# Kernel optimization log

Hardware: AMD Instinct MI355X
Metric: run time of the kernel (lower is better)

The kernel has to match this reference:

```python
import jax, jax.numpy as jnp
import numpy as np

N_NODES = 50000
N_EDGES = 800000
NEG_SLOPE = 0.2  # PyG GATConv default negative_slope


def gat_conv(x, W, att_src, att_dst, bias, src, dst, heads, out_ch, concat):
    """PyG GATConv (eval mode, self-loops already appended to src/dst)."""
    n = x.shape[0]
    xh = (x @ W).reshape(n, heads, out_ch)            # [N,H,C]
    a_s = jnp.einsum('nhc,hc->nh', xh, att_src)       # [N,H]
    a_d = jnp.einsum('nhc,hc->nh', xh, att_dst)
    e = a_s[src] + a_d[dst]                           # [E,H]
    e = jnp.where(e > 0, e, NEG_SLOPE * e)            # LeakyReLU
    # segment softmax over incoming edges of each target node (dst)
    m = jax.ops.segment_max(e, dst, num_segments=n)
    e = jnp.exp(e - m[dst])
    denom = jax.ops.segment_sum(e, dst, num_segments=n)
    alpha = e / (denom[dst] + 1e-16)                  # [E,H]
    msg = xh[src] * alpha[:, :, None]                 # [E,H,C]
    out = jax.ops.segment_sum(msg, dst, num_segments=n)  # [N,H,C]
    out = out.reshape(n, heads * out_ch) if concat else out.mean(axis=1)
    return out + bias


def setup_inputs() -> dict:
    key = jax.random.key(0)
    ks = jax.random.split(key, 16)
    x = jax.random.normal(ks[0], (N_NODES, 256), dtype=jnp.float32)
    edge_index = jax.random.randint(ks[1], (2, N_EDGES), 0, N_NODES, dtype=jnp.int32)
    s = 0.05
    return {
        'x': x, 'edge_index': edge_index,
        'W0': jax.random.normal(ks[2], (256, 256), jnp.float32) * s,
        'as0': jax.random.normal(ks[3], (4, 64), jnp.float32) * s,
        'ad0': jax.random.normal(ks[4], (4, 64), jnp.float32) * s,
        'b0': jnp.zeros((256,), jnp.float32),
        'W1': jax.random.normal(ks[5], (256, 256), jnp.float32) * s,
        'as1': jax.random.normal(ks[6], (4, 64), jnp.float32) * s,
        'ad1': jax.random.normal(ks[7], (4, 64), jnp.float32) * s,
        'b1': jnp.zeros((256,), jnp.float32),
        'W2': jax.random.normal(ks[8], (256, 256), jnp.float32) * s,
        'as2': jax.random.normal(ks[9], (1, 256), jnp.float32) * s,
        'ad2': jax.random.normal(ks[10], (1, 256), jnp.float32) * s,
        'b2': jnp.zeros((256,), jnp.float32),
    }


def reference(x, edge_index, W0, as0, ad0, b0, W1, as1, ad1, b1, W2, as2, ad2, b2):
    # PyG GATConv adds self-loops by default
    loops = jnp.arange(x.shape[0], dtype=edge_index.dtype)
    src = jnp.concatenate([edge_index[0], loops])
    dst = jnp.concatenate([edge_index[1], loops])
    h = jax.nn.elu(gat_conv(x, W0, as0, ad0, b0, src, dst, 4, 64, True))
    h = jax.nn.elu(gat_conv(h, W1, as1, ad1, b1, src, dst, 4, 64, True))
    return gat_conv(h, W2, as2, ad2, b2, src, dst, 1, 256, False)
```

## Files before the change

kernel.cpp:

```cpp
#include <hip/hip_runtime.h>
#include <hip/hip_bf16.h>
#include <hip/hip_fp16.h>

#define N_NODES 50000
#define N_EDGES 800000
#define E_TOTAL (N_EDGES + N_NODES)
#define BKT 96

typedef _Float16 f16x8 __attribute__((ext_vector_type(8)));
typedef _Float16 f16x4 __attribute__((ext_vector_type(4)));
typedef float f32x4 __attribute__((ext_vector_type(4)));

__device__ __forceinline__ void gl_lds16(const _Float16* g, _Float16* l) {
  __builtin_amdgcn_global_load_lds(
      (const __attribute__((address_space(1))) unsigned int*)g,
      (__attribute__((address_space(3))) unsigned int*)l, 16, 0, 0);
}

#define XCAST_BLK (N_NODES * 256 / 8 / 256)
#define EDGE_BLK ((E_TOTAL + 255) / 256)
__global__ __launch_bounds__(256) void prep_kernel(
    const float* __restrict__ W0, const float* __restrict__ W1,
    const float* __restrict__ W2, const float* __restrict__ x,
    const int* __restrict__ ei, _Float16* __restrict__ WT0,
    _Float16* __restrict__ WT1, _Float16* __restrict__ WT2,
    _Float16* __restrict__ X16, int* __restrict__ cursor,
    int* __restrict__ csr_src) {
  __shared__ float tile[32][33];
  const int bid = blockIdx.x;
  if (bid < 192) {
    const float* W = (bid < 64) ? W0 : (bid < 128) ? W1 : W2;
    _Float16* WT = (bid < 64) ? WT0 : (bid < 128) ? WT1 : WT2;
    const int sub = bid & 63;
    const int bx = (sub & 7) * 32, by = (sub >> 3) * 32;
    const int tx = threadIdx.x & 31, ty = threadIdx.x >> 5;
#pragma unroll
    for (int i = 0; i < 32; i += 8)
      tile[ty + i][tx] = W[(size_t)(by + ty + i) * 256 + bx + tx];
    __syncthreads();
#pragma unroll
    for (int i = 0; i < 32; i += 8)
      WT[(size_t)(bx + ty + i) * 256 + by + tx] = (_Float16)tile[tx][ty + i];
  } else if (bid < 192 + XCAST_BLK) {
    size_t i = ((size_t)(bid - 192) * 256 + threadIdx.x) * 8;
    float4 u0 = *(const float4*)(x + i);
    float4 u1 = *(const float4*)(x + i + 4);
    f16x8 v;
    v[0] = (_Float16)u0.x; v[1] = (_Float16)u0.y;
    v[2] = (_Float16)u0.z; v[3] = (_Float16)u0.w;
    v[4] = (_Float16)u1.x; v[5] = (_Float16)u1.y;
    v[6] = (_Float16)u1.z; v[7] = (_Float16)u1.w;
    *(f16x8*)(X16 + i) = v;
  } else {
    int e = (bid - 192 - XCAST_BLK) * 256 + threadIdx.x;
    if (e < E_TOTAL) {
      int s, d;
      if (e < N_EDGES) {
        s = ei[e];
        d = ei[N_EDGES + e];
      } else {
        s = d = e - N_EDGES;
      }
      int pos = atomicAdd(&cursor[d], 1);
      csr_src[(size_t)d * BKT + pos] = s;
    }
  }
}

template <int H>
__global__ __launch_bounds__(256) void gemm_att(
    const _Float16* __restrict__ A, const _Float16* __restrict__ WT,
    const float* __restrict__ att_s, const float* __restrict__ att_d,
    _Float16* __restrict__ C, float* __restrict__ a_s, float* __restrict__ a_d,
    int M) {
  __shared__ _Float16 As[2][64 * 32];
  __shared__ _Float16 Bs[2][256 * 32];
  const int t = threadIdx.x, lane = t & 63, w = t >> 6;
  const int wr = w & 1, wc = w >> 1;
  const int row0 = blockIdx.x * 64;
  const int fr = lane & 15, fg = lane >> 4;
  const int srow = lane >> 2, sk = (lane & 3) * 8;

  f32x4 acc[2][8] = {};
  int cur = 0;

#define STAGE(buf, k0)                                                        \
  do {                                                                        \
    gl_lds16(A + (size_t)(row0 + w * 16 + srow) * 256 + (k0) + sk,            \
             &As[buf][w * 512]);                                              \
    gl_lds16(WT + (size_t)(w * 64 + srow) * 256 + (k0) + sk,                  \
             &Bs[buf][w * 2048]);                                             \
    gl_lds16(WT + (size_t)(w * 64 + 16 + srow) * 256 + (k0) + sk,             \
             &Bs[buf][w * 2048 + 512]);                                       \
    gl_lds16(WT + (size_t)(w * 64 + 32 + srow) * 256 + (k0) + sk,             \
             &Bs[buf][w * 2048 + 1024]);                                      \
    gl_lds16(WT + (size_t)(w * 64 + 48 + srow) * 256 + (k0) + sk,             \
             &Bs[buf][w * 2048 + 1536]);                                      \
  } while (0)

  STAGE(0, 0);
  __syncthreads();

  for (int kt = 0; kt < 8; kt++) {
    if (kt < 7) STAGE(cur ^ 1, (kt + 1) * 32);
    f16x8 af[2], bf[8];
#pragma unroll
    for (int mi = 0; mi < 2; mi++)
      af[mi] = *(const f16x8*)&As[cur][(wr * 32 + mi * 16 + fr) * 32 + fg * 8];
#pragma unroll
    for (int ni = 0; ni < 8; ni++)
      bf[ni] = *(const f16x8*)&Bs[cur][(wc * 128 + ni * 16 + fr) * 32 + fg * 8];
#pragma unroll
    for (int mi = 0; mi < 2; mi++)
#pragma unroll
      for (int ni = 0; ni < 8; ni++)
        acc[mi][ni] = __builtin_amdgcn_mfma_f32_16x16x32_f16(af[mi], bf[ni], acc[mi][ni], 0, 0, 0);
    __syncthreads();
    cur ^= 1;
  }
#undef STAGE

  float as_c[8], ad_c[8];
#pragma unroll
  for (int ni = 0; ni < 8; ni++) {
    int c = wc * 128 + ni * 16 + fr;
    as_c[ni] = att_s[c];
    ad_c[ni] = att_d[c];
  }

#pragma unroll
  for (int mi = 0; mi < 2; mi++) {
#pragma unroll
    for (int reg = 0; reg < 4; reg++) {
      const int r = row0 + wr * 32 + mi * 16 + fg * 4 + reg;
      const bool valid = r < M;
      if (valid) {
#pragma unroll
        for (int ni = 0; ni < 8; ni++)
          C[(size_t)r * 256 + wc * 128 + ni * 16 + fr] = (_Float16)acc[mi][ni][reg];
      }
      float s0 = 0.f, s1 = 0.f, d0 = 0.f, d1 = 0.f;
#pragma unroll
      for (int ni = 0; ni < 4; ni++) {
        s0 = fmaf(acc[mi][ni][reg], as_c[ni], s0);
        d0 = fmaf(acc[mi][ni][reg], ad_c[ni], d0);
        s1 = fmaf(acc[mi][ni + 4][reg], as_c[ni + 4], s1);
        d1 = fmaf(acc[mi][ni + 4][reg], ad_c[ni + 4], d1);
      }
#pragma unroll
      for (int off = 1; off < 16; off <<= 1) {
        s0 += __shfl_xor(s0, off, 64);
        d0 += __shfl_xor(d0, off, 64);
        s1 += __shfl_xor(s1, off, 64);
        d1 += __shfl_xor(d1, off, 64);
      }
      if constexpr (H == 4) {
        if (fr == 0 && valid) {
          a_s[(size_t)r * 4 + wc * 2 + 0] = s0;
          a_s[(size_t)r * 4 + wc * 2 + 1] = s1;
          a_d[(size_t)r * 4 + wc * 2 + 0] = d0;
          a_d[(size_t)r * 4 + wc * 2 + 1] = d1;
        }
      } else {
        if (fr == 0) {
          float* L = (float*)As;
          L[(r - row0) * 4 + wc * 2 + 0] = s0 + s1;
          L[(r - row0) * 4 + wc * 2 + 1] = d0 + d1;
        }
      }
    }
  }
  if constexpr (H == 1) {
    __syncthreads();
    float* L = (float*)As;
    if (t < 64 && row0 + t < M) {
      a_s[row0 + t] = L[t * 4 + 0] + L[t * 4 + 2];
      a_d[row0 + t] = L[t * 4 + 1] + L[t * 4 + 3];
    }
  }
}

template <int H, bool ELU_OUT, bool OUT_F16>
__global__ __launch_bounds__(256, 8) void aggregate_kernel(
    const _Float16* __restrict__ XH16, const float* __restrict__ a_s,
    const float* __restrict__ a_d, const int* __restrict__ cursor,
    const int* __restrict__ csr_src, const float* __restrict__ bias,
    void* __restrict__ outp) {
  const int t = threadIdx.x;
  const int lane = t & 63, w = t >> 6;
  const int d = blockIdx.x * 4 + w;
  const size_t e0 = (size_t)d * BKT;
  const int deg = cursor[d];
  const int li = lane & 15;
  const int h4 = (H == 4) ? (lane >> 4) : 0;
  const float adv = (H == 4) ? a_d[(size_t)d * 4 + h4] : a_d[d];

  float dnp = 0.f;
  float acc0 = 0.f, acc1 = 0.f, acc2 = 0.f, acc3 = 0.f;
  for (int base = 0; base < deg; base += 16) {
    const int cnt = min(16, deg - base);
    int s_cur = 0;
    float p = 0.f;
    if (li < cnt) {
      s_cur = csr_src[e0 + base + li];
      float e = ((H == 4) ? a_s[(size_t)s_cur * 4 + h4] : a_s[s_cur]) + adv;
      e = e > 0.f ? e : 0.2f * e;
      p = __expf(e);
    }
    dnp += p;
#define GAT_BODY(j)                                                           \
  {                                                                           \
    int sj = __builtin_amdgcn_readfirstlane(__shfl(s_cur, (j), 64));          \
    float alj = __shfl(p, (lane & 48) + (j), 64);                             \
    f16x4 raw = *(const f16x4*)(XH16 + (size_t)sj * 256 + lane * 4);          \
    acc0 = fmaf(alj, (float)raw[0], acc0);                                    \
    acc1 = fmaf(alj, (float)raw[1], acc1);                                    \
    acc2 = fmaf(alj, (float)raw[2], acc2);                                    \
    acc3 = fmaf(alj, (float)raw[3], acc3);                                    \
  }
    if (cnt == 16) {
#pragma unroll
      for (int j = 0; j < 16; j++) GAT_BODY(j)
    } else {
      for (int j = 0; j < cnt; j++) GAT_BODY(j)
    }
#undef GAT_BODY
  }
#pragma unroll
  for (int off = 1; off < 16; off <<= 1) dnp += __shfl_xor(dnp, off, 64);
  const float inv = 1.f / (dnp + 1e-16f);

  float4 bv = *(const float4*)&bias[lane * 4];
  float v0 = fmaf(acc0, inv, bv.x), v1 = fmaf(acc1, inv, bv.y);
  float v2 = fmaf(acc2, inv, bv.z), v3 = fmaf(acc3, inv, bv.w);
  if constexpr (ELU_OUT) {
    v0 = v0 > 0.f ? v0 : (__expf(v0) - 1.f);
    v1 = v1 > 0.f ? v1 : (__expf(v1) - 1.f);
    v2 = v2 > 0.f ? v2 : (__expf(v2) - 1.f);
    v3 = v3 > 0.f ? v3 : (__expf(v3) - 1.f);
  }
  if constexpr (OUT_F16) {
    _Float16* out = (_Float16*)outp;
    f16x4 ov;
    ov[0] = (_Float16)v0; ov[1] = (_Float16)v1;
    ov[2] = (_Float16)v2; ov[3] = (_Float16)v3;
    *(f16x4*)(out + (size_t)d * 256 + lane * 4) = ov;
  } else {
    float* out = (float*)outp;
    *(float4*)(out + (size_t)d * 256 + lane * 4) = make_float4(v0, v1, v2, v3);
  }
}

extern "C" void kernel_launch(void* const* d_in, const int* in_sizes, int n_in,
                              void* d_out, int out_size, void* d_ws, size_t ws_size,
                              hipStream_t stream) {
  const float* x = (const float*)d_in[0];
  const int* ei = (const int*)d_in[1];
  const float* W0 = (const float*)d_in[2];
  const float* as0 = (const float*)d_in[3];
  const float* ad0 = (const float*)d_in[4];
  const float* b0 = (const float*)d_in[5];
  const float* W1 = (const float*)d_in[6];
  const float* as1 = (const float*)d_in[7];
  const float* ad1 = (const float*)d_in[8];
  const float* b1 = (const float*)d_in[9];
  const float* W2 = (const float*)d_in[10];
  const float* as2 = (const float*)d_in[11];
  const float* ad2 = (const float*)d_in[12];
  const float* b2 = (const float*)d_in[13];
  float* out = (float*)d_out;

  char* p = (char*)d_ws;
  _Float16* XH16 = (_Float16*)p;
  p += (size_t)N_NODES * 256 * 2;
  _Float16* H16 = (_Float16*)p;
  p += (size_t)N_NODES * 256 * 2;
  _Float16* WT0 = (_Float16*)p;
  p += 256 * 256 * 2;
  _Float16* WT1 = (_Float16*)p;
  p += 256 * 256 * 2;
  _Float16* WT2 = (_Float16*)p;
  p += 256 * 256 * 2;
  float* a_s = (float*)p;
  p += (size_t)N_NODES * 4 * 4;
  float* a_d = (float*)p;
  p += (size_t)N_NODES * 4 * 4;
  int* cursor = (int*)p;
  p += (size_t)N_NODES * 4;
  int* csr_src = (int*)p;
  p += (size_t)N_NODES * BKT * 4;

  hipMemsetAsync(cursor, 0, (size_t)N_NODES * 4, stream);

  prep_kernel<<<192 + XCAST_BLK + EDGE_BLK, 256, 0, stream>>>(
      W0, W1, W2, x, ei, WT0, WT1, WT2, H16, cursor, csr_src);

  const int ggrid = (N_NODES + 63) / 64;
  const int ngrid = N_NODES / 4;

  gemm_att<4><<<ggrid, 256, 0, stream>>>(H16, WT0, as0, ad0, XH16, a_s, a_d, N_NODES);
  aggregate_kernel<4, true, true><<<ngrid, 256, 0, stream>>>(XH16, a_s, a_d, cursor, csr_src, b0, H16);
  gemm_att<4><<<ggrid, 256, 0, stream>>>(H16, WT1, as1, ad1, XH16, a_s, a_d, N_NODES);
  aggregate_kernel<4, true, true><<<ngrid, 256, 0, stream>>>(XH16, a_s, a_d, cursor, csr_src, b1, H16);
  gemm_att<1><<<ggrid, 256, 0, stream>>>(H16, WT2, as2, ad2, XH16, a_s, a_d, N_NODES);
  aggregate_kernel<1, false, false><<<ngrid, 256, 0, stream>>>(XH16, a_s, a_d, cursor, csr_src, b2, out);
}
```

Baseline: 371.0 us.

## Move CSR edge scatter into first GEMM launch and store sources as 16-bit

```diff
diff --git a/kernel.cpp b/kernel.cpp
--- a/kernel.cpp
+++ b/kernel.cpp
@@ -6,6 +6,9 @@
 #define N_EDGES 800000
 #define E_TOTAL (N_EDGES + N_NODES)
 #define BKT 96
+#define NTILES 782
+#define XCAST_BLK (N_NODES * 256 / 8 / 256)
+#define EDGE_BLK ((E_TOTAL + 255) / 256)
 
 typedef _Float16 f16x8 __attribute__((ext_vector_type(8)));
 typedef _Float16 f16x4 __attribute__((ext_vector_type(4)));
@@ -17,15 +20,11 @@
       (__attribute__((address_space(3))) unsigned int*)l, 16, 0, 0);
 }
 
-#define XCAST_BLK (N_NODES * 256 / 8 / 256)
-#define EDGE_BLK ((E_TOTAL + 255) / 256)
 __global__ __launch_bounds__(256) void prep_kernel(
     const float* __restrict__ W0, const float* __restrict__ W1,
     const float* __restrict__ W2, const float* __restrict__ x,
-    const int* __restrict__ ei, _Float16* __restrict__ WT0,
-    _Float16* __restrict__ WT1, _Float16* __restrict__ WT2,
-    _Float16* __restrict__ X16, int* __restrict__ cursor,
-    int* __restrict__ csr_src) {
+    _Float16* __restrict__ WT0, _Float16* __restrict__ WT1,
+    _Float16* __restrict__ WT2, _Float16* __restrict__ X16) {
   __shared__ float tile[32][33];
   const int bid = blockIdx.x;
   if (bid < 192) {
@@ -41,7 +40,7 @@
 #pragma unroll
     for (int i = 0; i < 32; i += 8)
       WT[(size_t)(bx + ty + i) * 256 + by + tx] = (_Float16)tile[tx][ty + i];
-  } else if (bid < 192 + XCAST_BLK) {
+  } else {
     size_t i = ((size_t)(bid - 192) * 256 + threadIdx.x) * 8;
     float4 u0 = *(const float4*)(x + i);
     float4 u1 = *(const float4*)(x + i + 4);
@@ -51,33 +50,40 @@
     v[4] = (_Float16)u1.x; v[5] = (_Float16)u1.y;
     v[6] = (_Float16)u1.z; v[7] = (_Float16)u1.w;
     *(f16x8*)(X16 + i) = v;
-  } else {
-    int e = (bid - 192 - XCAST_BLK) * 256 + threadIdx.x;
-    if (e < E_TOTAL) {
-      int s, d;
-      if (e < N_EDGES) {
-        s = ei[e];
-        d = ei[N_EDGES + e];
-      } else {
-        s = d = e - N_EDGES;
-      }
-      int pos = atomicAdd(&cursor[d], 1);
-      csr_src[(size_t)d * BKT + pos] = s;
-    }
-  }
-}
-
-template <int H>
+  }
+}
+
+template <int H, bool SCAT>
 __global__ __launch_bounds__(256) void gemm_att(
     const _Float16* __restrict__ A, const _Float16* __restrict__ WT,
     const float* __restrict__ att_s, const float* __restrict__ att_d,
     _Float16* __restrict__ C, float* __restrict__ a_s, float* __restrict__ a_d,
-    int M) {
+    int M, const int* __restrict__ ei, int* __restrict__ cursor,
+    unsigned short* __restrict__ csr_src) {
   __shared__ _Float16 As[2][64 * 32];
   __shared__ _Float16 Bs[2][256 * 32];
+  int bid = blockIdx.x;
+  if constexpr (SCAT) {
+    if (bid < EDGE_BLK) {
+      int e = bid * 256 + threadIdx.x;
+      if (e < E_TOTAL) {
+        int s, d;
+        if (e < N_EDGES) {
+          s = ei[e];
+          d = ei[N_EDGES + e];
+        } else {
+          s = d = e - N_EDGES;
+        }
+        int pos = atomicAdd(&cursor[d], 1);
+        csr_src[(size_t)d * BKT + pos] = (unsigned short)s;
+      }
+      return;
+    }
+    bid -= EDGE_BLK;
+  }
   const int t = threadIdx.x, lane = t & 63, w = t >> 6;
   const int wr = w & 1, wc = w >> 1;
-  const int row0 = blockIdx.x * 64;
+  const int row0 = bid * 64;
   const int fr = lane & 15, fg = lane >> 4;
   const int srow = lane >> 2, sk = (lane & 3) * 8;
 
@@ -184,7 +190,7 @@
 __global__ __launch_bounds__(256, 8) void aggregate_kernel(
     const _Float16* __restrict__ XH16, const float* __restrict__ a_s,
     const float* __restrict__ a_d, const int* __restrict__ cursor,
-    const int* __restrict__ csr_src, const float* __restrict__ bias,
+    const unsigned short* __restrict__ csr_src, const float* __restrict__ bias,
     void* __restrict__ outp) {
   const int t = threadIdx.x;
   const int lane = t & 63, w = t >> 6;
@@ -287,21 +293,26 @@
   p += (size_t)N_NODES * 4 * 4;
   int* cursor = (int*)p;
   p += (size_t)N_NODES * 4;
-  int* csr_src = (int*)p;
-  p += (size_t)N_NODES * BKT * 4;
+  unsigned short* csr_src = (unsigned short*)p;
+  p += (size_t)N_NODES * BKT * 2;
 
   hipMemsetAsync(cursor, 0, (size_t)N_NODES * 4, stream);
 
-  prep_kernel<<<192 + XCAST_BLK + EDGE_BLK, 256, 0, stream>>>(
-      W0, W1, W2, x, ei, WT0, WT1, WT2, H16, cursor, csr_src);
-
-  const int ggrid = (N_NODES + 63) / 64;
+  prep_kernel<<<192 + XCAST_BLK, 256, 0, stream>>>(W0, W1, W2, x, WT0, WT1,
+                                                   WT2, H16);
+
   const int ngrid = N_NODES / 4;
 
-  gemm_att<4><<<ggrid, 256, 0, stream>>>(H16, WT0, as0, ad0, XH16, a_s, a_d, N_NODES);
-  aggregate_kernel<4, true, true><<<ngrid, 256, 0, stream>>>(XH16, a_s, a_d, cursor, csr_src, b0, H16);
-  gemm_att<4><<<ggrid, 256, 0, stream>>>(H16, WT1, as1, ad1, XH16, a_s, a_d, N_NODES);
-  aggregate_kernel<4, true, true><<<ngrid, 256, 0, stream>>>(XH16, a_s, a_d, cursor, csr_src, b1, H16);
-  gemm_att<1><<<ggrid, 256, 0, stream>>>(H16, WT2, as2, ad2, XH16, a_s, a_d, N_NODES);
-  aggregate_kernel<1, false, false><<<ngrid, 256, 0, stream>>>(XH16, a_s, a_d, cursor, csr_src, b2, out);
-}
+  gemm_att<4, true><<<EDGE_BLK + NTILES, 256, 0, stream>>>(
+      H16, WT0, as0, ad0, XH16, a_s, a_d, N_NODES, ei, cursor, csr_src);
+  aggregate_kernel<4, true, true><<<ngrid, 256, 0, stream>>>(
+      XH16, a_s, a_d, cursor, csr_src, b0, H16);
+  gemm_att<4, false><<<NTILES, 256, 0, stream>>>(
+      H16, WT1, as1, ad1, XH16, a_s, a_d, N_NODES, ei, cursor, csr_src);
+  aggregate_kernel<4, true, true><<<ngrid, 256, 0, stream>>>(
+      XH16, a_s, a_d, cursor, csr_src, b1, H16);
+  gemm_att<1, false><<<NTILES, 256, 0, stream>>>(
+      H16, WT2, as2, ad2, XH16, a_s, a_d, N_NODES, ei, cursor, csr_src);
+  aggregate_kernel<1, false, false><<<ngrid, 256, 0, stream>>>(
+      XH16, a_s, a_d, cursor, csr_src, b2, out);
+}
```

Measured after the change: 362.4 us. 2.3% less time.
